# Kernel optimization log

Measured on AMD Instinct MI355X. Metric: run time of the kernel, lower is better.

Reference implementation:

```python
import jax, jax.numpy as jnp
import numpy as np


def setup_inputs() -> dict:
    key = jax.random.key(0)
    k1, k2, k3, k4 = jax.random.split(key, 4)
    B, T, E, D = 4, 4096, 2048, 128
    x = jax.random.normal(k1, (B, T, E), dtype=jnp.float32)
    # nn.Linear(E, D, bias=False): y = x @ W where W is [E, D]
    scale = 1.0 / np.sqrt(E)
    Wq = jax.random.normal(k2, (E, D), dtype=jnp.float32) * scale
    Wk = jax.random.normal(k3, (E, D), dtype=jnp.float32) * scale
    Wv = jax.random.normal(k4, (E, D), dtype=jnp.float32) * scale
    return {"x": x, "Wq": Wq, "Wk": Wk, "Wv": Wv}


def reference(x, Wq, Wk, Wv):
    # Single attention head, prefill path (kv_cache=None, T_q == T_k).
    D = Wq.shape[1]
    Q = jnp.einsum('bte,ed->btd', x, Wq)
    K = jnp.einsum('bte,ed->btd', x, Wk)
    V = jnp.einsum('bte,ed->btd', x, Wv)
    scores = jnp.einsum('bqd,bkd->bqk', Q, K) / jnp.sqrt(jnp.float32(D))
    T = x.shape[1]
    causal = jnp.tril(jnp.ones((T, T), dtype=bool))  # [T_q, T_k]
    scores = jnp.where(causal[None, :, :], scores, -jnp.inf)
    attn = jax.nn.softmax(scores, axis=-1)
    out = jnp.einsum('bqk,bkd->bqd', attn, V)
    return out
```

## Files before the change

### kernel.cpp

```cpp
#include <hip/hip_runtime.h>
#include <hip/hip_bf16.h>

typedef short bf16x8 __attribute__((ext_vector_type(8)));
typedef float f32x4  __attribute__((ext_vector_type(4)));

#define T_SEQ 4096
#define NB    4
#define E_DIM 2048
#define D_DIM 128
#define M_TOT (NB * T_SEQ)
#define NCHUNK 4
#define CHUNK_KT 16
#define SM_SHIFT 12.0f

__device__ __forceinline__ ushort f2bf(float f) {
  union { float f; unsigned u; } c; c.f = f;
  unsigned u = c.u;
  unsigned r = (u + 0x7FFFu + ((u >> 16) & 1u)) >> 16;
  return (ushort)r;
}
__device__ __forceinline__ float bf2f(ushort u) {
  union { unsigned u; float f; } c; c.u = ((unsigned)u) << 16;
  return c.f;
}
__device__ __forceinline__ bf16x8 cvt8(const float4& lo, const float4& hi) {
  union { __hip_bfloat162 h; ushort u[2]; } t;
  union { ushort u[8]; bf16x8 v; } r;
  t.h = __float22bfloat162_rn(make_float2(lo.x, lo.y)); r.u[0] = t.u[0]; r.u[1] = t.u[1];
  t.h = __float22bfloat162_rn(make_float2(lo.z, lo.w)); r.u[2] = t.u[0]; r.u[3] = t.u[1];
  t.h = __float22bfloat162_rn(make_float2(hi.x, hi.y)); r.u[4] = t.u[0]; r.u[5] = t.u[1];
  t.h = __float22bfloat162_rn(make_float2(hi.z, hi.w)); r.u[6] = t.u[0]; r.u[7] = t.u[1];
  return r.v;
}

__device__ __forceinline__ void gl2lds16(const void* g, void* l) {
  __builtin_amdgcn_global_load_lds(
      (const __attribute__((address_space(1))) unsigned int*)g,
      (__attribute__((address_space(3))) unsigned int*)l, 16, 0, 0);
}

__global__ __launch_bounds__(256) void build_wt(const float* __restrict__ Wq,
                                                const float* __restrict__ Wk,
                                                const float* __restrict__ Wv,
                                                ushort* __restrict__ Wt) {
  __shared__ ushort tile[64][72];
  const int tid = threadIdx.x;
  const int k0 = blockIdx.x * 64, n0 = blockIdx.y * 64, o = blockIdx.z;
  const float* W = (o == 0) ? Wq : ((o == 1) ? Wk : Wv);
  for (int i = 0; i < 4; i++) {
    int c = tid + i * 256;
    int r = c >> 4, c4 = (c & 15) * 4;
    float4 v = *(const float4*)(W + (size_t)(k0 + r) * D_DIM + n0 + c4);
    ushort4 b4;
    b4.x = f2bf(v.x); b4.y = f2bf(v.y); b4.z = f2bf(v.z); b4.w = f2bf(v.w);
    *(ushort4*)(&tile[r][c4]) = b4;
  }
  __syncthreads();
  for (int i = 0; i < 2; i++) {
    int c = tid + i * 256;
    int nn = c >> 3, k8 = (c & 7) * 8;
    ushort tmp[8];
    for (int j = 0; j < 8; j++) tmp[j] = tile[k8 + j][nn];
    *(uint4*)(Wt + (size_t)((o << 7) + n0 + nn) * E_DIM + k0 + k8) = *(const uint4*)tmp;
  }
}

__global__ __launch_bounds__(256) void qkv_gemm(const float* __restrict__ x,
                                                const ushort* __restrict__ Wt,
                                                ushort* __restrict__ Q,
                                                ushort* __restrict__ K,
                                                ushort* __restrict__ V) {
  __shared__ ushort Bs[2][192 * 64];

  const int tid  = threadIdx.x;
  const int wave = tid >> 6, lane = tid & 63;
  const int quad = lane >> 4, l16 = lane & 15;
  const int wm = wave >> 1, wn = wave & 1;
  const int m0 = blockIdx.x * 64;
  const int n0 = blockIdx.y * 192;

  f32x4 acc[2][6] = {};

  const int s_   = wave * 64 + lane;
  const int n_   = s_ >> 3, p_ = s_ & 7;

#define DMA_B(k0_, buf_)                                                        \
  for (int i_ = 0; i_ < 6; i_++) {                                              \
    int slotbase = i_ * 256 + wave * 64;                                        \
    int n = (i_ * 256 >> 3) + n_;       \
    int cg = p_ ^ (n & 7);                                                      \
    gl2lds16(Wt + (size_t)(n0 + n) * E_DIM + (k0_) + cg * 8,                    \
             (char*)(buf_) + (size_t)slotbase * 16);                            \
  }

  DMA_B(0, Bs[0]);
  __syncthreads();

  const float* xbase = x + (size_t)(m0 + wm * 32 + l16) * E_DIM + quad * 8;

  for (int it = 0; it < 32; it++) {
    const int k0 = it * 64;
    if (it < 31) { DMA_B(k0 + 64, Bs[(it + 1) & 1]); }
    const ushort* bs = Bs[it & 1];

    float4 a4[2][2][2];
    for (int mi = 0; mi < 2; mi++)
      for (int kk = 0; kk < 2; kk++) {
        const float* ap = xbase + (size_t)mi * 16 * E_DIM + k0 + kk * 32;
        a4[mi][kk][0] = *(const float4*)ap;
        a4[mi][kk][1] = *(const float4*)(ap + 4);
      }

    for (int kk = 0; kk < 2; kk++) {
      bf16x8 af[2];
      af[0] = cvt8(a4[0][kk][0], a4[0][kk][1]);
      af[1] = cvt8(a4[1][kk][0], a4[1][kk][1]);
      const int sw = ((kk * 4 + quad) ^ (l16 & 7)) * 8;
      for (int ni = 0; ni < 6; ni++) {
        int n = wn * 96 + ni * 16 + l16;
        bf16x8 bf = *(const bf16x8*)(bs + n * 64 + sw);
        acc[0][ni] = __builtin_amdgcn_mfma_f32_16x16x32_bf16(af[0], bf, acc[0][ni], 0, 0, 0);
        acc[1][ni] = __builtin_amdgcn_mfma_f32_16x16x32_bf16(af[1], bf, acc[1][ni], 0, 0, 0);
      }
    }
    __syncthreads();
  }

  for (int mi = 0; mi < 2; mi++)
    for (int ni = 0; ni < 6; ni++) {
      int colall = n0 + wn * 96 + ni * 16 + l16;
      int o = colall >> 7, d = colall & 127;
      ushort* dst = (o == 0) ? Q : ((o == 1) ? K : V);
      for (int r = 0; r < 4; r++) {
        int row = m0 + wm * 32 + mi * 16 + quad * 4 + r;
        dst[(size_t)row * D_DIM + d] = f2bf(acc[mi][ni][r]);
      }
    }
#undef DMA_B
}

__global__ __launch_bounds__(256) void v_transpose(const ushort* __restrict__ V,
                                                   ushort* __restrict__ Vt) {
  __shared__ ushort tile[64][72];
  const int tid = threadIdx.x;
  const int t0 = blockIdx.x * 64, d0 = blockIdx.y * 64, b = blockIdx.z;
  for (int i = 0; i < 2; i++) {
    int c = tid + i * 256;
    int r = c >> 3, cc = (c & 7) * 8;
    *(uint4*)(&tile[r][cc]) = *(const uint4*)(V + (size_t)(b * T_SEQ + t0 + r) * D_DIM + d0 + cc);
  }
  __syncthreads();
  for (int i = 0; i < 2; i++) {
    int c = tid + i * 256;
    int dr = c >> 3, tc = (c & 7) * 8;
    ushort tmp[8];
    for (int j = 0; j < 8; j++) tmp[j] = tile[tc + j][dr];
    *(uint4*)(Vt + (size_t)(b * D_DIM + d0 + dr) * T_SEQ + t0 + tc) = *(const uint4*)tmp;
  }
}

__global__ __launch_bounds__(256) void attn_partial(const ushort* __restrict__ Q,
                                                    const ushort* __restrict__ K,
                                                    const ushort* __restrict__ Vt,
                                                    ushort* __restrict__ Po,
                                                    float* __restrict__ Ll) {
  const int qt = blockIdx.x, cq = blockIdx.y, b = blockIdx.z;
  const int kt0 = cq * CHUNK_KT;
  if (kt0 > qt) return;

  __shared__ ushort Kt[64][136];
  __shared__ ushort Vts[128][72];
  __shared__ ushort Pls[4][16][72];

  const int tid = threadIdx.x;
  const int wave = tid >> 6, lane = tid & 63;
  const int quad = lane >> 4, l16 = lane & 15;

  const int qrow = qt * 64 + wave * 16 + l16;
  bf16x8 qf[4];
  for (int kk = 0; kk < 4; kk++)
    qf[kk] = *(const bf16x8*)(Q + (size_t)(b * T_SEQ + qrow) * D_DIM + kk * 32 + quad * 8);

  bf16x8 ones;
  for (int j = 0; j < 8; j++) ones[j] = (short)0x3F80;

  f32x4 o_acc[8] = {};
  f32x4 lacc = {};
  const float scale2 = 0.08838834764831845f * 1.4426950408889634f;

  const int kt1 = min(qt, kt0 + CHUNK_KT - 1);

  for (int kt = kt0; kt <= kt1; kt++) {
    __syncthreads();
    for (int i = 0; i < 4; i++) {
      int c = tid + i * 256;
      int r = c >> 4, col = (c & 15) * 8;
      *(uint4*)(&Kt[r][col]) = *(const uint4*)(K + (size_t)(b * T_SEQ + kt * 64 + r) * D_DIM + col);
    }
    for (int i = 0; i < 4; i++) {
      int c = tid + i * 256;
      int dr = c >> 3, col = (c & 7) * 8;
      *(uint4*)(&Vts[dr][col]) = *(const uint4*)(Vt + (size_t)(b * D_DIM + dr) * T_SEQ + kt * 64 + col);
    }
    __syncthreads();

    f32x4 s[4] = {};
    for (int kk = 0; kk < 4; kk++) {
      const int kc = kk * 32 + quad * 8;
      for (int ni = 0; ni < 4; ni++) {
        bf16x8 bf = *(const bf16x8*)(&Kt[ni * 16 + l16][kc]);
        s[ni] = __builtin_amdgcn_mfma_f32_16x16x32_bf16(qf[kk], bf, s[ni], 0, 0, 0);
      }
    }
    if (kt == qt) {
      for (int ni = 0; ni < 4; ni++) {
        int kidx = kt * 64 + ni * 16 + l16;
        for (int r = 0; r < 4; r++) {
          int qidx = qt * 64 + wave * 16 + quad * 4 + r;
          float v = (kidx > qidx) ? -1e30f : (s[ni][r] * scale2 - SM_SHIFT);
          s[ni][r] = exp2f(v);
        }
      }
    } else {
      for (int ni = 0; ni < 4; ni++)
        for (int r = 0; r < 4; r++)
          s[ni][r] = exp2f(s[ni][r] * scale2 - SM_SHIFT);
    }
    for (int ni = 0; ni < 4; ni++)
      for (int r = 0; r < 4; r++)
        Pls[wave][quad * 4 + r][ni * 16 + l16] = f2bf(s[ni][r]);
    for (int kk2 = 0; kk2 < 2; kk2++) {
      const int kc = kk2 * 32 + quad * 8;
      bf16x8 pf = *(const bf16x8*)(&Pls[wave][l16][kc]);
      for (int ni = 0; ni < 8; ni++) {
        bf16x8 vf = *(const bf16x8*)(&Vts[ni * 16 + l16][kc]);
        o_acc[ni] = __builtin_amdgcn_mfma_f32_16x16x32_bf16(pf, vf, o_acc[ni], 0, 0, 0);
      }
      lacc = __builtin_amdgcn_mfma_f32_16x16x32_bf16(pf, ones, lacc, 0, 0, 0);
    }
  }

  const int slot = (b * 64 + qt) * NCHUNK + cq;
  for (int ni = 0; ni < 8; ni++)
    for (int r = 0; r < 4; r++) {
      int ql = wave * 16 + quad * 4 + r;
      Po[(size_t)slot * 8192 + ql * D_DIM + ni * 16 + l16] = f2bf(o_acc[ni][r]);
    }
  if (l16 == 0) {
    for (int r = 0; r < 4; r++) {
      int ql = wave * 16 + quad * 4 + r;
      Ll[slot * 64 + ql] = lacc[r];
    }
  }
}

__global__ __launch_bounds__(256) void attn_reduce(const ushort* __restrict__ Po,
                                                   const float* __restrict__ Ll,
                                                   float* __restrict__ out) {
  const int qt = blockIdx.x, b = blockIdx.y;
  const int nc = qt / CHUNK_KT + 1;
  const int tid = threadIdx.x;
  const int row = tid >> 2;
  const int c0  = (tid & 3) * 32;
  const int base_slot = (b * 64 + qt) * NCHUNK;

  float L = 0.f;
  for (int c = 0; c < nc; c++) L += Ll[(base_slot + c) * 64 + row];
  const float inv = 1.0f / L;

  const size_t orow = (size_t)(b * T_SEQ + qt * 64 + row) * D_DIM;
  for (int cc = 0; cc < 32; cc += 8) {
    float a[8] = {0,0,0,0,0,0,0,0};
    for (int c = 0; c < nc; c++) {
      const ushort* p = Po + (size_t)(base_slot + c) * 8192 + row * D_DIM + c0 + cc;
      ushort u[8];
      *(uint4*)u = *(const uint4*)p;
      for (int j = 0; j < 8; j++) a[j] += bf2f(u[j]);
    }
    float4 o0, o1;
    o0.x = a[0] * inv; o0.y = a[1] * inv; o0.z = a[2] * inv; o0.w = a[3] * inv;
    o1.x = a[4] * inv; o1.y = a[5] * inv; o1.z = a[6] * inv; o1.w = a[7] * inv;
    *(float4*)(out + orow + c0 + cc)     = o0;
    *(float4*)(out + orow + c0 + cc + 4) = o1;
  }
}

extern "C" void kernel_launch(void* const* d_in, const int* in_sizes, int n_in,
                              void* d_out, int out_size, void* d_ws, size_t ws_size,
                              hipStream_t stream) {
  const float* x  = (const float*)d_in[0];
  const float* Wq = (const float*)d_in[1];
  const float* Wk = (const float*)d_in[2];
  const float* Wv = (const float*)d_in[3];
  float* out = (float*)d_out;

  ushort* Q  = (ushort*)d_ws;
  ushort* Kb = Q  + (size_t)M_TOT * D_DIM;
  ushort* Vb = Kb + (size_t)M_TOT * D_DIM;
  ushort* Vt = Vb + (size_t)M_TOT * D_DIM;
  ushort* Wt = Vt + (size_t)M_TOT * D_DIM;
  ushort* Po = Wt + (size_t)384 * E_DIM;
  float*  Ll = (float*)(Po + (size_t)NB * 64 * NCHUNK * 8192);

  hipLaunchKernelGGL(build_wt,     dim3(32, 2, 3),       dim3(256), 0, stream, Wq, Wk, Wv, Wt);
  hipLaunchKernelGGL(qkv_gemm,     dim3(256, 2),         dim3(256), 0, stream, x, Wt, Q, Kb, Vb);
  hipLaunchKernelGGL(v_transpose,  dim3(64, 2, 4),       dim3(256), 0, stream, Vb, Vt);
  hipLaunchKernelGGL(attn_partial, dim3(64, NCHUNK, 4),  dim3(256), 0, stream, Q, Kb, Vt, Po, Ll);
  hipLaunchKernelGGL(attn_reduce,  dim3(64, 4),          dim3(256), 0, stream, Po, Ll, out);
}
```

Baseline: 299.9 us.

## Prefetch x tiles one iteration ahead and swap QKV GEMM grid order

The QKV GEMM now loads the next k-step of fp32 x rows into registers while the current step's MFMAs run, instead of loading and consuming them in the same iteration. The grid is also transposed so the two N-tiles that share the same x rows are launched next to each other, which should improve L2 reuse of the large x input. The cost is extra VGPRs for the double-buffered A fragments, which could lower occupancy.

```diff
diff --git a/kernel.cpp b/kernel.cpp
--- a/kernel.cpp
+++ b/kernel.cpp
@@ -76,8 +76,8 @@
   const int wave = tid >> 6, lane = tid & 63;
   const int quad = lane >> 4, l16 = lane & 15;
   const int wm = wave >> 1, wn = wave & 1;
-  const int m0 = blockIdx.x * 64;
-  const int n0 = blockIdx.y * 192;
+  const int m0 = blockIdx.y * 64;
+  const int n0 = blockIdx.x * 192;
 
   f32x4 acc[2][6] = {};
 
@@ -93,28 +93,33 @@
              (char*)(buf_) + (size_t)slotbase * 16);                            \
   }
 
+#define LOAD_A(k0_, dst)                                                        \
+  for (int mi_ = 0; mi_ < 2; mi_++)                                             \
+    for (int kk_ = 0; kk_ < 2; kk_++) {                                         \
+      const float* ap_ = xbase + (size_t)mi_ * 16 * E_DIM + (k0_) + kk_ * 32;   \
+      dst[mi_][kk_][0] = *(const float4*)ap_;                                   \
+      dst[mi_][kk_][1] = *(const float4*)(ap_ + 4);                             \
+    }
+
+  const float* xbase = x + (size_t)(m0 + wm * 32 + l16) * E_DIM + quad * 8;
+
+  float4 aCur[2][2][2], aNxt[2][2][2];
   DMA_B(0, Bs[0]);
+  LOAD_A(0, aCur);
   __syncthreads();
-
-  const float* xbase = x + (size_t)(m0 + wm * 32 + l16) * E_DIM + quad * 8;
 
   for (int it = 0; it < 32; it++) {
     const int k0 = it * 64;
-    if (it < 31) { DMA_B(k0 + 64, Bs[(it + 1) & 1]); }
+    if (it < 31) {
+      DMA_B(k0 + 64, Bs[(it + 1) & 1]);
+      LOAD_A(k0 + 64, aNxt);
+    }
     const ushort* bs = Bs[it & 1];
-
-    float4 a4[2][2][2];
-    for (int mi = 0; mi < 2; mi++)
-      for (int kk = 0; kk < 2; kk++) {
-        const float* ap = xbase + (size_t)mi * 16 * E_DIM + k0 + kk * 32;
-        a4[mi][kk][0] = *(const float4*)ap;
-        a4[mi][kk][1] = *(const float4*)(ap + 4);
-      }
 
     for (int kk = 0; kk < 2; kk++) {
       bf16x8 af[2];
-      af[0] = cvt8(a4[0][kk][0], a4[0][kk][1]);
-      af[1] = cvt8(a4[1][kk][0], a4[1][kk][1]);
+      af[0] = cvt8(aCur[0][kk][0], aCur[0][kk][1]);
+      af[1] = cvt8(aCur[1][kk][0], aCur[1][kk][1]);
       const int sw = ((kk * 4 + quad) ^ (l16 & 7)) * 8;
       for (int ni = 0; ni < 6; ni++) {
         int n = wn * 96 + ni * 16 + l16;
@@ -124,6 +129,15 @@
       }
     }
     __syncthreads();
+    if (it < 31) {
+#pragma unroll
+      for (int mi = 0; mi < 2; mi++)
+#pragma unroll
+        for (int kk = 0; kk < 2; kk++) {
+          aCur[mi][kk][0] = aNxt[mi][kk][0];
+          aCur[mi][kk][1] = aNxt[mi][kk][1];
+        }
+    }
   }
 
   for (int mi = 0; mi < 2; mi++)
@@ -137,6 +151,7 @@
       }
     }
 #undef DMA_B
+#undef LOAD_A
 }
 
 __global__ __launch_bounds__(256) void v_transpose(const ushort* __restrict__ V,
@@ -303,7 +318,7 @@
   float*  Ll = (float*)(Po + (size_t)NB * 64 * NCHUNK * 8192);
 
   hipLaunchKernelGGL(build_wt,     dim3(32, 2, 3),       dim3(256), 0, stream, Wq, Wk, Wv, Wt);
-  hipLaunchKernelGGL(qkv_gemm,     dim3(256, 2),         dim3(256), 0, stream, x, Wt, Q, Kb, Vb);
+  hipLaunchKernelGGL(qkv_gemm,     dim3(2, 256),         dim3(256), 0, stream, x, Wt, Q, Kb, Vb);
   hipLaunchKernelGGL(v_transpose,  dim3(64, 2, 4),       dim3(256), 0, stream, Vb, Vt);
   hipLaunchKernelGGL(attn_partial, dim3(64, NCHUNK, 4),  dim3(256), 0, stream, Q, Kb, Vt, Po, Ll);
   hipLaunchKernelGGL(attn_reduce,  dim3(64, 4),          dim3(256), 0, stream, Po, Ll, out);
```

Result: slower. 310.4 us (+3.5%).

## Software-pipeline QKV projection with double-buffered A registers and manual waitcnts

Applied to the files above, without the earlier changes.

Restructures the QKV projection GEMM main loop into a two-stage unrolled pipeline. The x (A operand) loads for the next k-step are issued into a second register buffer alongside the weight DMA into LDS, and explicit s_waitcnt vmcnt values replace __syncthreads so compute on the current tile overlaps with outstanding global loads. This targets global-load latency stalls in the projection kernel, which is only one part of the whole pipeline. In exchange it raises register pressure, and correctness now depends on hand-counted vmcnt values matching the number of loads issued.

```diff
diff --git a/kernel.cpp b/kernel.cpp
--- a/kernel.cpp
+++ b/kernel.cpp
@@ -85,6 +85,7 @@
   const int n_   = s_ >> 3, p_ = s_ & 7;
 
 #define DMA_B(k0_, buf_)                                                        \
+  _Pragma("unroll")                                                             \
   for (int i_ = 0; i_ < 6; i_++) {                                              \
     int slotbase = i_ * 256 + wave * 64;                                        \
     int n = (i_ * 256 >> 3) + n_;       \
@@ -93,37 +94,61 @@
              (char*)(buf_) + (size_t)slotbase * 16);                            \
   }
 
+#define LOAD_A(k0_, dst)                                                        \
+  _Pragma("unroll")                                                             \
+  for (int mi_ = 0; mi_ < 2; mi_++)                                             \
+    _Pragma("unroll")                                                           \
+    for (int kk_ = 0; kk_ < 2; kk_++) {                                         \
+      const float* ap_ = xbase + (size_t)mi_ * 16 * E_DIM + (k0_) + kk_ * 32;   \
+      dst[mi_][kk_][0] = *(const float4*)ap_;                                   \
+      dst[mi_][kk_][1] = *(const float4*)(ap_ + 4);                             \
+    }
+
+#define COMPUTE(aBuf, bufidx)                                                   \
+  {                                                                             \
+    const ushort* bs = Bs[bufidx];                                              \
+    _Pragma("unroll")                                                           \
+    for (int kk = 0; kk < 2; kk++) {                                            \
+      bf16x8 af0 = cvt8(aBuf[0][kk][0], aBuf[0][kk][1]);                        \
+      bf16x8 af1 = cvt8(aBuf[1][kk][0], aBuf[1][kk][1]);                        \
+      const int sw = ((kk * 4 + quad) ^ (l16 & 7)) * 8;                         \
+      _Pragma("unroll")                                                         \
+      for (int ni = 0; ni < 6; ni++) {                                          \
+        int n = wn * 96 + ni * 16 + l16;                                        \
+        bf16x8 bf = *(const bf16x8*)(bs + n * 64 + sw);                         \
+        acc[0][ni] = __builtin_amdgcn_mfma_f32_16x16x32_bf16(af0, bf, acc[0][ni], 0, 0, 0); \
+        acc[1][ni] = __builtin_amdgcn_mfma_f32_16x16x32_bf16(af1, bf, acc[1][ni], 0, 0, 0); \
+      }                                                                         \
+    }                                                                           \
+  }
+
+  const float* xbase = x + (size_t)(m0 + wm * 32 + l16) * E_DIM + quad * 8;
+
+  float4 a0[2][2][2], a1[2][2][2];
+
   DMA_B(0, Bs[0]);
-  __syncthreads();
-
-  const float* xbase = x + (size_t)(m0 + wm * 32 + l16) * E_DIM + quad * 8;
-
-  for (int it = 0; it < 32; it++) {
-    const int k0 = it * 64;
-    if (it < 31) { DMA_B(k0 + 64, Bs[(it + 1) & 1]); }
-    const ushort* bs = Bs[it & 1];
-
-    float4 a4[2][2][2];
-    for (int mi = 0; mi < 2; mi++)
-      for (int kk = 0; kk < 2; kk++) {
-        const float* ap = xbase + (size_t)mi * 16 * E_DIM + k0 + kk * 32;
-        a4[mi][kk][0] = *(const float4*)ap;
-        a4[mi][kk][1] = *(const float4*)(ap + 4);
-      }
-
-    for (int kk = 0; kk < 2; kk++) {
-      bf16x8 af[2];
-      af[0] = cvt8(a4[0][kk][0], a4[0][kk][1]);
-      af[1] = cvt8(a4[1][kk][0], a4[1][kk][1]);
-      const int sw = ((kk * 4 + quad) ^ (l16 & 7)) * 8;
-      for (int ni = 0; ni < 6; ni++) {
-        int n = wn * 96 + ni * 16 + l16;
-        bf16x8 bf = *(const bf16x8*)(bs + n * 64 + sw);
-        acc[0][ni] = __builtin_amdgcn_mfma_f32_16x16x32_bf16(af[0], bf, acc[0][ni], 0, 0, 0);
-        acc[1][ni] = __builtin_amdgcn_mfma_f32_16x16x32_bf16(af[1], bf, acc[1][ni], 0, 0, 0);
-      }
-    }
-    __syncthreads();
+  LOAD_A(0, a0);
+  asm volatile("s_waitcnt vmcnt(0) lgkmcnt(0)" ::: "memory");
+  __builtin_amdgcn_s_barrier();
+
+  for (int it = 0; it < 32; it += 2) {
+    DMA_B((it + 1) * 64, Bs[1]);
+    LOAD_A((it + 1) * 64, a1);
+    asm volatile("s_waitcnt vmcnt(14)" ::: "memory");
+    COMPUTE(a0, 0);
+    asm volatile("s_waitcnt vmcnt(8) lgkmcnt(0)" ::: "memory");
+    __builtin_amdgcn_s_barrier();
+    if (it < 30) {
+      DMA_B((it + 2) * 64, Bs[0]);
+      LOAD_A((it + 2) * 64, a0);
+      asm volatile("s_waitcnt vmcnt(14)" ::: "memory");
+      COMPUTE(a1, 1);
+      asm volatile("s_waitcnt vmcnt(8) lgkmcnt(0)" ::: "memory");
+      __builtin_amdgcn_s_barrier();
+    } else {
+      asm volatile("s_waitcnt vmcnt(0) lgkmcnt(0)" ::: "memory");
+      COMPUTE(a1, 1);
+    }
   }
 
   for (int mi = 0; mi < 2; mi++)
@@ -137,6 +162,8 @@
       }
     }
 #undef DMA_B
+#undef LOAD_A
+#undef COMPUTE
 }
 
 __global__ __launch_bounds__(256) void v_transpose(const ushort* __restrict__ V,
```

New measurement: 305.8 us. About the same (+2.0%).
